# Performance work log

Hardware: AMD Instinct MI355X
Metric: run time of the kernel (lower is better)

Reference implementation:

```python
import jax, jax.numpy as jnp
import numpy as np

N_PTS = 600000; N_VOX = 250000; N_PART = 125000; N_NEXT = 100000; N_DS = 100000
C = 64; K = 27; B = 2; SX, SY, SZ = 240, 180, 16


def leaky(x):
    return jnp.where(x >= 0, x, 0.1 * x)


def bn(x, g, b, eps=1e-5):
    # training-mode BatchNorm1d: batch stats over the row dim
    mu = x.mean(0)
    var = x.var(0)
    return (x - mu) * jax.lax.rsqrt(var + eps) * g + b


def subm_conv(x, nbr, W):
    # submanifold 3x3x3 conv via precomputed neighbor map: [N,K] gather + per-offset GEMM
    return jnp.einsum('nkc,kcd->nd', x[nbr], W)


def basic_block(x, nbr, W1, g1, b1, W2, g2, b2):
    h = leaky(bn(subm_conv(x, nbr, W1), g1, b1))
    h = bn(subm_conv(h, nbr, W2), g2, b2)
    return leaky(h + x)


def scatter_mean(x, idx, n):
    s = jax.ops.segment_sum(x, idx, num_segments=n)
    cnt = jax.ops.segment_sum(jnp.ones((x.shape[0], 1), x.dtype), idx, num_segments=n)
    return s / jnp.maximum(cnt, 1.0)


def forward(feats, feats_part, Wv11, g11, b11, Wv12, g12, b12, Wv21, g21, b21, Wv22, g22, b22, Wlog, blog, Wi, bi, Wp1, bp1, gp1, bp1n, Wp2, bp2, gp2, bp2n, Wp3, bp3, Wo1, bo1, Wo2, bo2, nbr, nbr_part, coors, coors_inv_last, coors_inv_next, ds_inv):
    # v_enc: two SparseBasicBlocks (shared weights for full and partial tensors)
    v = basic_block(basic_block(feats, nbr, Wv11, g11, b11, Wv12, g12, b12), nbr, Wv21, g21, b21, Wv22, g22, b22)
    vp = basic_block(basic_block(feats_part, nbr_part, Wv11, g11, b11, Wv12, g12, b12), nbr_part, Wv21, g21, b21, Wv22, g22, b22)
    # mae logits on partial tensor + dense BCEWithLogits against all-ones occupancy
    logit = subm_conv(vp, nbr_part, Wlog) + blog  # [N_PART, 1]
    ncell = B * SX * SY * SZ
    flat = ((coors[:, 0] * SX + coors[:, 1]) * SY + coors[:, 2]) * SZ + coors[:, 3]
    x_dense = jnp.zeros((ncell,), feats.dtype).at[flat[:N_PART]].set(logit[:, 0])
    t_dense = jnp.zeros((ncell,), feats.dtype).at[flat].set(1.0)
    loss = jnp.mean(jnp.maximum(x_dense, 0.0) - x_dense * t_dense + jnp.log1p(jnp.exp(-jnp.abs(x_dense))))
    # point_encoder on sparse feats + voxel feats
    feat_sum = feats + v
    ds = scatter_mean(feat_sum, ds_inv, N_DS)           # downsample via unique-inverse
    identity = leaky(feat_sum @ Wi + bi)                # layer_in
    h = bn(leaky(ds @ Wp1 + bp1), gp1, bp1n)            # PPmodel
    h = bn(leaky(h @ Wp2 + bp2), gp2, bp2n)
    h = leaky(h @ Wp3 + bp3)
    cat = jnp.concatenate([identity, h[ds_inv]], axis=1)  # [N_VOX, 2C]
    g = cat[coors_inv_last]                             # gather to points [N_PTS, 2C]
    lo = leaky(g @ Wo1 + bo1) @ Wo2 + bo2               # layer_out
    p_fea = scatter_mean(lo, coors_inv_next, N_NEXT)    # [N_NEXT, C]
    return p_fea[coors_inv_next], loss


def setup_inputs():
    key = jax.random.key(0)
    ks = iter(jax.random.split(key, 48))
    f32 = jnp.float32
    def rn(shape, s):
        return jax.random.normal(next(ks), shape, f32) * s
    def ri(shape, hi):
        return jax.random.randint(next(ks), shape, 0, hi, jnp.int32)
    d = {}
    d['feats'] = rn((N_VOX, C), 1.0)
    d['feats_part'] = rn((N_PART, C), 1.0)
    for nm in ('Wv11', 'Wv12', 'Wv21', 'Wv22'):
        d[nm] = rn((K, C, C), 0.02)
    for nm in ('g11', 'g12', 'g21', 'g22'):
        d[nm] = jnp.ones((C,), f32)
    for nm in ('b11', 'b12', 'b21', 'b22'):
        d[nm] = jnp.zeros((C,), f32)
    d['Wlog'] = rn((K, C, 1), 0.02); d['blog'] = jnp.zeros((1,), f32)
    d['Wi'] = rn((C, C), 0.1); d['bi'] = jnp.zeros((C,), f32)
    d['Wp1'] = rn((C, C // 2), 0.1); d['bp1'] = jnp.zeros((C // 2,), f32)
    d['gp1'] = jnp.ones((C // 2,), f32); d['bp1n'] = jnp.zeros((C // 2,), f32)
    d['Wp2'] = rn((C // 2, C // 2), 0.15); d['bp2'] = jnp.zeros((C // 2,), f32)
    d['gp2'] = jnp.ones((C // 2,), f32); d['bp2n'] = jnp.zeros((C // 2,), f32)
    d['Wp3'] = rn((C // 2, C), 0.15); d['bp3'] = jnp.zeros((C,), f32)
    d['Wo1'] = rn((2 * C, C), 0.08); d['bo1'] = jnp.zeros((C,), f32)
    d['Wo2'] = rn((C, C), 0.1); d['bo2'] = jnp.zeros((C,), f32)
    d['nbr'] = ri((N_VOX, K), N_VOX)
    d['nbr_part'] = ri((N_PART, K), N_PART)
    d['coors'] = jnp.stack([ri((N_VOX,), B), ri((N_VOX,), SX), ri((N_VOX,), SY), ri((N_VOX,), SZ)], axis=1)
    d['coors_inv_last'] = ri((N_PTS,), N_VOX)
    d['coors_inv_next'] = ri((N_PTS,), N_NEXT)
    d['ds_inv'] = ri((N_VOX,), N_DS)
    return d


def reference(feats, feats_part, Wv11, g11, b11, Wv12, g12, b12, Wv21, g21, b21, Wv22, g22, b22, Wlog, blog, Wi, bi, Wp1, bp1, gp1, bp1n, Wp2, bp2, gp2, bp2n, Wp3, bp3, Wo1, bo1, Wo2, bo2, nbr, nbr_part, coors, coors_inv_last, coors_inv_next, ds_inv):
    return forward(feats, feats_part, Wv11, g11, b11, Wv12, g12, b12, Wv21, g21, b21, Wv22, g22, b22, Wlog, blog, Wi, bi, Wp1, bp1, gp1, bp1n, Wp2, bp2, gp2, bp2n, Wp3, bp3, Wo1, bo1, Wo2, bo2, nbr, nbr_part, coors, coors_inv_last, coors_inv_next, ds_inv)
```

## Files before the change

### kernel.cpp

```cpp
#include <hip/hip_runtime.h>
#include <math.h>

#define NVOX 250000
#define NPART 125000
#define NPTS 600000
#define NNEXT 100000
#define NDS 100000
#define NCELL 1382400

static __device__ __forceinline__ float lk(float x) { return x >= 0.f ? x : 0.1f * x; }

static __device__ __forceinline__ unsigned short f2bf(float f) {
    unsigned u = __float_as_uint(f);
    unsigned r = (u + 0x7FFFu + ((u >> 16) & 1u)) >> 16;
    return (unsigned short)r;
}
static __device__ __forceinline__ unsigned short f2h(float f) {
    _Float16 h = (_Float16)f;
    return *(unsigned short*)&h;
}
static __device__ __forceinline__ float h2f(unsigned short u) {
    _Float16 h = *(_Float16*)&u;
    return (float)h;
}

typedef short v8s __attribute__((ext_vector_type(8)));
typedef _Float16 v8h __attribute__((ext_vector_type(8)));
typedef float v4f __attribute__((ext_vector_type(4)));
#define MFMAH __builtin_amdgcn_mfma_f32_16x16x32_f16

static __device__ __forceinline__ float* lob_row(float* r0, float* r1, float* r2, int row) {
    if (row < 200000) return r0 + (size_t)row * 64;
    if (row < 500000) return r1 + (size_t)(row - 200000) * 64;
    return r2 + (size_t)(row - 500000) * 64;
}

__global__ void fill_u32_kernel(unsigned* __restrict__ p, unsigned v, long n) {
    long i = (long)blockIdx.x * 256 + threadIdx.x;
    if (i < n) p[i] = v;
}

__global__ void wsplit_kernel(const float* __restrict__ W, unsigned short* __restrict__ hi,
                              unsigned short* __restrict__ lo) {
    int i = blockIdx.x * 256 + threadIdx.x;
    if (i < 27 * 4096) {
        int k = i >> 12, rem = i & 4095, d = rem >> 6, c = rem & 63;
        float w = W[k * 4096 + c * 64 + d];
        unsigned short h = f2h(w);
        hi[i] = h;
        lo[i] = f2h(w - h2f(h));
    }
}

__global__ void xhalf_kernel(const float* __restrict__ X, unsigned short* __restrict__ out, long n) {
    long i = (long)blockIdx.x * 256 + threadIdx.x;
    if (i < n) out[i] = f2h(X[i]);
}

__global__ __launch_bounds__(256) void conv_mfma_kernel(
    const unsigned short* __restrict__ Xh,
    const int* __restrict__ nbr,
    const unsigned short* __restrict__ Wthi, const unsigned short* __restrict__ Wtlo,
    float* __restrict__ Y, float* __restrict__ stats, int N)
{
    __shared__ __align__(16) unsigned short Wlds[2][8192];

    const int t = threadIdx.x;
    const int wave = t >> 6, lane = t & 63;
    const int m = lane & 15, q = lane >> 4;
    const int qo = q * 8;
    const long base = (long)blockIdx.x * 128 + wave * 32;

    long r0 = base + m;
    long r1 = base + 16 + m;
    long r0c = r0 < N ? r0 : (long)(N - 1);
    long r1c = r1 < N ? r1 : (long)(N - 1);
    const long o0g = r0c * 27, o1g = r1c * 27;

    const int zb = wave * 4096 + lane * 16;
    const int z0 = zb, z1 = zb + 1024, z2 = zb + 2048, z3 = zb + 3072;
    const int d0 = z0 ^ (((z0 >> 7) & 7) << 4);
    const int d1 = z1 ^ (((z1 >> 7) & 7) << 4);
    const int d2 = z2 ^ (((z2 >> 7) & 7) << 4);
    const int d3 = z3 ^ (((z3 >> 7) & 7) << 4);

    v4f acc[2][4];
    #pragma unroll
    for (int s = 0; s < 2; ++s)
        #pragma unroll
        for (int c = 0; c < 4; ++c)
            acc[s][c] = (v4f){0.f, 0.f, 0.f, 0.f};

    {
        const char* ghb = (const char*)Wthi;
        const char* glb = (const char*)Wtlo;
        v8s w0 = *(const v8s*)(z0 < 8192 ? ghb + z0 : glb + (z0 - 8192));
        v8s w1 = *(const v8s*)(z1 < 8192 ? ghb + z1 : glb + (z1 - 8192));
        v8s w2 = *(const v8s*)(z2 < 8192 ? ghb + z2 : glb + (z2 - 8192));
        v8s w3 = *(const v8s*)(z3 < 8192 ? ghb + z3 : glb + (z3 - 8192));
        char* lb = (char*)&Wlds[0][0];
        *(v8s*)(lb + d0) = w0; *(v8s*)(lb + d1) = w1;
        *(v8s*)(lb + d2) = w2; *(v8s*)(lb + d3) = w3;
    }
    __syncthreads();

    #pragma unroll 1
    for (int k = 0; k < 27; ++k) {
        const int cb = k & 1;
        const bool st = (k + 1 < 27);
        v8s w0, w1, w2, w3;
        if (st) {
            const char* ghb = (const char*)(Wthi + (size_t)(k + 1) * 4096);
            const char* glb = (const char*)(Wtlo + (size_t)(k + 1) * 4096);
            w0 = *(const v8s*)(z0 < 8192 ? ghb + z0 : glb + (z0 - 8192));
            w1 = *(const v8s*)(z1 < 8192 ? ghb + z1 : glb + (z1 - 8192));
            w2 = *(const v8s*)(z2 < 8192 ? ghb + z2 : glb + (z2 - 8192));
            w3 = *(const v8s*)(z3 < 8192 ? ghb + z3 : glb + (z3 - 8192));
        }
        int j0 = nbr[o0g + k];
        int j1 = nbr[o1g + k];
        const unsigned short* x0 = Xh + (size_t)j0 * 64;
        const unsigned short* x1 = Xh + (size_t)j1 * 64;
        v8h a00 = *(const v8h*)(x0 + qo);
        v8h a01 = *(const v8h*)(x0 + 32 + qo);
        v8h a10 = *(const v8h*)(x1 + qo);
        v8h a11 = *(const v8h*)(x1 + 32 + qo);
        const char* wb = (const char*)&Wlds[cb][0];
        const int sw = (m & 7) << 4;
        #pragma unroll
        for (int ct = 0; ct < 4; ++ct) {
            const int rowoff = (ct * 16 + m) * 128;
            v8h bh0 = *(const v8h*)(wb + rowoff + ((q * 16) ^ sw));
            v8h bh1 = *(const v8h*)(wb + rowoff + ((q * 16 + 64) ^ sw));
            v8h bl0 = *(const v8h*)(wb + 8192 + rowoff + ((q * 16) ^ sw));
            v8h bl1 = *(const v8h*)(wb + 8192 + rowoff + ((q * 16 + 64) ^ sw));
            acc[0][ct] = MFMAH(a00, bh0, acc[0][ct], 0, 0, 0);
            acc[0][ct] = MFMAH(a01, bh1, acc[0][ct], 0, 0, 0);
            acc[0][ct] = MFMAH(a00, bl0, acc[0][ct], 0, 0, 0);
            acc[0][ct] = MFMAH(a01, bl1, acc[0][ct], 0, 0, 0);
            acc[1][ct] = MFMAH(a10, bh0, acc[1][ct], 0, 0, 0);
            acc[1][ct] = MFMAH(a11, bh1, acc[1][ct], 0, 0, 0);
            acc[1][ct] = MFMAH(a10, bl0, acc[1][ct], 0, 0, 0);
            acc[1][ct] = MFMAH(a11, bl1, acc[1][ct], 0, 0, 0);
        }
        if (st) {
            char* lb = (char*)&Wlds[1 - cb][0];
            *(v8s*)(lb + d0) = w0; *(v8s*)(lb + d1) = w1;
            *(v8s*)(lb + d2) = w2; *(v8s*)(lb + d3) = w3;
        }
        __syncthreads();
    }

    #pragma unroll
    for (int s = 0; s < 2; ++s)
        #pragma unroll
        for (int ct = 0; ct < 4; ++ct)
            #pragma unroll
            for (int rg = 0; rg < 4; ++rg) {
                long r = base + s * 16 + q * 4 + rg;
                if (r < N) Y[r * 64 + ct * 16 + m] = acc[s][ct][rg];
            }

    float* shred = (float*)&Wlds[0][0];
    if (t < 128) shred[t] = 0.f;
    __syncthreads();
    #pragma unroll
    for (int ct = 0; ct < 4; ++ct) {
        float s = 0.f, s2 = 0.f;
        #pragma unroll
        for (int ss = 0; ss < 2; ++ss)
            #pragma unroll
            for (int rg = 0; rg < 4; ++rg) {
                long r = base + ss * 16 + q * 4 + rg;
                if (r < N) { float v = acc[ss][ct][rg]; s += v; s2 += v * v; }
            }
        atomicAdd(&shred[ct * 16 + m], s);
        atomicAdd(&shred[64 + ct * 16 + m], s2);
    }
    __syncthreads();
    if (t < 64) {
        atomicAdd(&stats[t], shred[t]);
        atomicAdd(&stats[64 + t], shred[64 + t]);
    }
}

template<int CC>
__global__ __launch_bounds__(256) void colstats_kernel(const float* __restrict__ Y, int N, float* __restrict__ stats) {
    constexpr int RG = 256 / CC;
    const int t = threadIdx.x;
    const int c = t % CC, rg = t / CC;
    float s = 0.f, s2 = 0.f;
    for (long r = (long)blockIdx.x * RG + rg; r < N; r += (long)gridDim.x * RG) {
        float v = Y[r * CC + c];
        s += v; s2 += v * v;
    }
    __shared__ float sh[256], sh2[256];
    sh[t] = s; sh2[t] = s2;
    __syncthreads();
    if (t < CC) {
        #pragma unroll
        for (int g = 1; g < RG; ++g) { s += sh[g * CC + t]; s2 += sh2[g * CC + t]; }
        atomicAdd(&stats[t], s);
        atomicAdd(&stats[CC + t], s2);
    }
}

__global__ void mkscale_kernel(float* __restrict__ stats, const float* __restrict__ g,
                               const float* __restrict__ b, float invN, int CC) {
    int c = threadIdx.x;
    if (c < CC) {
        float mu = stats[c] * invN;
        float var = stats[CC + c] * invN - mu * mu;
        float sc = g[c] * rsqrtf(var + 1e-5f);
        stats[2 * CC + c] = sc;
        stats[3 * CC + c] = b[c] - mu * sc;
    }
}

template<int CC, int MODE, int PAIR, int WOUT>
__global__ __launch_bounds__(256) void apply_bn_kernel(
    const float* __restrict__ Yin, const float* __restrict__ stats,
    const float* __restrict__ res, const float* __restrict__ res2,
    float* __restrict__ out, unsigned short* __restrict__ ohalf, long n4)
{
    long i = (long)blockIdx.x * 256 + threadIdx.x;
    if (i >= n4) return;
    int c4 = (int)(i % (CC / 4)) * 4;
    float4 y = ((const float4*)Yin)[i];
    float4 sc = *(const float4*)(stats + 2 * CC + c4);
    float4 sf = *(const float4*)(stats + 3 * CC + c4);
    float x0 = y.x * sc.x + sf.x;
    float x1 = y.y * sc.y + sf.y;
    float x2 = y.z * sc.z + sf.z;
    float x3 = y.w * sc.w + sf.w;
    if (MODE >= 2) {
        float4 rr = ((const float4*)res)[i];
        x0 += rr.x; x1 += rr.y; x2 += rr.z; x3 += rr.w;
    }
    if (MODE >= 1) { x0 = lk(x0); x1 = lk(x1); x2 = lk(x2); x3 = lk(x3); }
    if (MODE == 3) {
        float4 rr2 = ((const float4*)res2)[i];
        x0 += rr2.x; x1 += rr2.y; x2 += rr2.z; x3 += rr2.w;
    }
    if (WOUT) ((float4*)out)[i] = make_float4(x0, x1, x2, x3);
    if (PAIR) {
        ushort4 h;
        h.x = f2h(x0); h.y = f2h(x1); h.z = f2h(x2); h.w = f2h(x3);
        *(ushort4*)(ohalf + i * 4) = h;
    }
}

template<int CIN, int COUT, int ACT>
__global__ __launch_bounds__(256) void gemm_kernel(
    const float* __restrict__ X, const float* __restrict__ W,
    const float* __restrict__ bias, float* __restrict__ Y, int N)
{
    constexpr int TX = COUT / 4;
    constexpr int TY = 256 / TX;
    constexpr int ROWS = TY * 4;
    constexpr int CHUNK = (CIN < 64) ? CIN : 64;
    constexpr int NCH = CIN / CHUNK;
    __shared__ float XsT[CHUNK][ROWS + 4];
    __shared__ float Ws[CHUNK][COUT + 4];
    const int t = threadIdx.x;
    const int row0 = blockIdx.x * ROWS;
    const int ty = t / TX, tx = t % TX;
    float acc[4][4] = {{0.f}};
    for (int cc = 0; cc < NCH; ++cc) {
        __syncthreads();
        for (int i = t * 4; i < CHUNK * COUT; i += 1024) {
            int c = i / COUT, d = i % COUT;
            *(float4*)&Ws[c][d] = *(const float4*)(W + (size_t)(cc * CHUNK + c) * COUT + d);
        }
        for (int i = t * 4; i < ROWS * CHUNK; i += 1024) {
            int r = i / CHUNK, c0 = i % CHUNK;
            int gr = row0 + r;
            float4 v = make_float4(0.f, 0.f, 0.f, 0.f);
            if (gr < N) v = *(const float4*)(X + (size_t)gr * CIN + cc * CHUNK + c0);
            XsT[c0 + 0][r] = v.x; XsT[c0 + 1][r] = v.y; XsT[c0 + 2][r] = v.z; XsT[c0 + 3][r] = v.w;
        }
        __syncthreads();
        #pragma unroll 8
        for (int c = 0; c < CHUNK; ++c) {
            float4 xv = *(const float4*)&XsT[c][ty * 4];
            float4 wv = *(const float4*)&Ws[c][tx * 4];
            acc[0][0] += xv.x * wv.x; acc[0][1] += xv.x * wv.y; acc[0][2] += xv.x * wv.z; acc[0][3] += xv.x * wv.w;
            acc[1][0] += xv.y * wv.x; acc[1][1] += xv.y * wv.y; acc[1][2] += xv.y * wv.z; acc[1][3] += xv.y * wv.w;
            acc[2][0] += xv.z * wv.x; acc[2][1] += xv.z * wv.y; acc[2][2] += xv.z * wv.z; acc[2][3] += xv.z * wv.w;
            acc[3][0] += xv.w * wv.x; acc[3][1] += xv.w * wv.y; acc[3][2] += xv.w * wv.z; acc[3][3] += xv.w * wv.w;
        }
    }
    float4 bv = *(const float4*)(bias + tx * 4);
    #pragma unroll
    for (int i2 = 0; i2 < 4; ++i2) {
        int gr = row0 + ty * 4 + i2;
        if (gr < N) {
            float o0 = acc[i2][0] + bv.x, o1 = acc[i2][1] + bv.y;
            float o2 = acc[i2][2] + bv.z, o3 = acc[i2][3] + bv.w;
            if (ACT) { o0 = lk(o0); o1 = lk(o1); o2 = lk(o2); o3 = lk(o3); }
            *(float4*)(Y + (size_t)gr * COUT + tx * 4) = make_float4(o0, o1, o2, o3);
        }
    }
}

__global__ void hist_kernel(const int* __restrict__ idx, int* __restrict__ cnt, int n) {
    int i = blockIdx.x * 256 + threadIdx.x;
    if (i < n) atomicAdd(&cnt[idx[i]], 1);
}

__global__ void scan_reduce_kernel(const int* __restrict__ cnt, int* __restrict__ bsum, int T) {
    __shared__ int sh[256];
    const int b = blockIdx.x, t = threadIdx.x;
    int s = 0;
    #pragma unroll
    for (int u = 0; u < 4; ++u) {
        int i = b * 1024 + u * 256 + t;
        if (i < T) s += cnt[i];
    }
    sh[t] = s; __syncthreads();
    for (int st = 128; st > 0; st >>= 1) { if (t < st) sh[t] += sh[t + st]; __syncthreads(); }
    if (t == 0) bsum[b] = sh[0];
}

__global__ void scan_top_kernel(int* __restrict__ bsum, int nb) {
    __shared__ int sh[256];
    const int t = threadIdx.x;
    sh[t] = (t < nb) ? bsum[t] : 0;
    __syncthreads();
    if (t == 0) {
        int run = 0;
        for (int i = 0; i < nb; ++i) { int v = sh[i]; sh[i] = run; run += v; }
    }
    __syncthreads();
    if (t < nb) bsum[t] = sh[t];
}

__global__ void scan_final_kernel(const int* __restrict__ cnt, const int* __restrict__ bsum,
                                  int* __restrict__ offs, int* __restrict__ cursor, int T) {
    __shared__ int sh[256];
    const int b = blockIdx.x, t = threadIdx.x;
    const int i0 = b * 1024 + t * 4;
    int v0 = 0, v1 = 0, v2 = 0, v3 = 0;
    if (i0 + 0 < T) v0 = cnt[i0 + 0];
    if (i0 + 1 < T) v1 = cnt[i0 + 1];
    if (i0 + 2 < T) v2 = cnt[i0 + 2];
    if (i0 + 3 < T) v3 = cnt[i0 + 3];
    const int tot = v0 + v1 + v2 + v3;
    sh[t] = tot; __syncthreads();
    for (int st = 1; st < 256; st <<= 1) {
        int x = (t >= st) ? sh[t - st] : 0;
        __syncthreads();
        sh[t] += x;
        __syncthreads();
    }
    int ex = sh[t] - tot + bsum[b];
    if (i0 + 0 < T) { offs[i0 + 0] = ex; cursor[i0 + 0] = ex; } ex += v0;
    if (i0 + 1 < T) { offs[i0 + 1] = ex; cursor[i0 + 1] = ex; } ex += v1;
    if (i0 + 2 < T) { offs[i0 + 2] = ex; cursor[i0 + 2] = ex; } ex += v2;
    if (i0 + 3 < T) { offs[i0 + 3] = ex; cursor[i0 + 3] = ex; }
}

__global__ void place_kernel(const int* __restrict__ idx, int* __restrict__ cursor,
                             int* __restrict__ perm, int n) {
    int i = blockIdx.x * 256 + threadIdx.x;
    if (i < n) { int p = atomicAdd(&cursor[idx[i]], 1); perm[p] = i; }
}

__global__ __launch_bounds__(256) void segmean_kernel(
    const float* __restrict__ src, const int* __restrict__ perm,
    const int* __restrict__ offs, const int* __restrict__ cnt,
    float* __restrict__ dst, int T)
{
    const int wave = threadIdx.x >> 6, lane = threadIdx.x & 63;
    const int tg = blockIdx.x * 4 + wave;
    if (tg >= T) return;
    const int o = offs[tg], c = cnt[tg];
    float acc = 0.f;
    for (int j = 0; j < c; ++j) {
        int r = perm[o + j];
        acc += src[(size_t)r * 64 + lane];
    }
    dst[(size_t)tg * 64 + lane] = acc / fmaxf((float)c, 1.0f);
}

__global__ __launch_bounds__(256) void segmean_lob_kernel(
    float* __restrict__ l0, float* __restrict__ l1, float* __restrict__ l2,
    const int* __restrict__ perm, const int* __restrict__ offs, const int* __restrict__ cnt,
    float* __restrict__ dst, int T)
{
    const int wave = threadIdx.x >> 6, lane = threadIdx.x & 63;
    const int tg = blockIdx.x * 4 + wave;
    if (tg >= T) return;
    const int o = offs[tg], c = cnt[tg];
    float acc = 0.f;
    for (int j = 0; j < c; ++j) {
        int r = perm[o + j];
        acc += lob_row(l0, l1, l2, r)[lane];
    }
    dst[(size_t)tg * 64 + lane] = acc / fmaxf((float)c, 1.0f);
}

__global__ __launch_bounds__(256) void layer_out_fused_kernel(
    const float* __restrict__ iden, const float* __restrict__ h3,
    const int* __restrict__ cil, const int* __restrict__ dsinv,
    const float* __restrict__ Wo1, const float* __restrict__ bo1,
    const float* __restrict__ Wo2, const float* __restrict__ bo2,
    float* __restrict__ lob0, float* __restrict__ lob1, float* __restrict__ lob2, int N)
{
    __shared__ float XsT[64][68];
    __shared__ float Ws[64][68];
    const int t = threadIdx.x;
    const int row0 = blockIdx.x * 64;
    const int ty = t >> 4, tx = t & 15;
    const int lr = t >> 2, ls = t & 3;
    const int gr = row0 + lr;
    int v = (gr < N) ? cil[gr] : 0;
    int vds = dsinv[v];
    float acc[4][4] = {{0.f}};
    for (int cc = 0; cc < 2; ++cc) {
        const float* src = (cc == 0) ? (iden + (size_t)v * 64) : (h3 + (size_t)vds * 64);
        const float* xr = src + ls * 16;
        float4 v0 = *(const float4*)(xr);
        float4 v1 = *(const float4*)(xr + 4);
        float4 v2f = *(const float4*)(xr + 8);
        float4 v3 = *(const float4*)(xr + 12);
        const float* Wk = Wo1 + (size_t)cc * 4096;
        float4 w0 = *(const float4*)(Wk + t * 4);
        float4 w1 = *(const float4*)(Wk + t * 4 + 1024);
        float4 w2 = *(const float4*)(Wk + t * 4 + 2048);
        float4 w3 = *(const float4*)(Wk + t * 4 + 3072);
        __syncthreads();
        {
            int i0 = t * 4;
            *(float4*)&Ws[i0 >> 6][i0 & 63] = w0; i0 += 1024;
            *(float4*)&Ws[i0 >> 6][i0 & 63] = w1; i0 += 1024;
            *(float4*)&Ws[i0 >> 6][i0 & 63] = w2; i0 += 1024;
            *(float4*)&Ws[i0 >> 6][i0 & 63] = w3;
        }
        const int cb = ls * 16;
        XsT[cb + 0][lr] = v0.x; XsT[cb + 1][lr] = v0.y; XsT[cb + 2][lr] = v0.z; XsT[cb + 3][lr] = v0.w;
        XsT[cb + 4][lr] = v1.x; XsT[cb + 5][lr] = v1.y; XsT[cb + 6][lr] = v1.z; XsT[cb + 7][lr] = v1.w;
        XsT[cb + 8][lr] = v2f.x; XsT[cb + 9][lr] = v2f.y; XsT[cb + 10][lr] = v2f.z; XsT[cb + 11][lr] = v2f.w;
        XsT[cb + 12][lr] = v3.x; XsT[cb + 13][lr] = v3.y; XsT[cb + 14][lr] = v3.z; XsT[cb + 15][lr] = v3.w;
        __syncthreads();
        #pragma unroll 16
        for (int c = 0; c < 64; ++c) {
            float4 xv = *(const float4*)&XsT[c][ty * 4];
            float4 wv = *(const float4*)&Ws[c][tx * 4];
            acc[0][0] += xv.x * wv.x; acc[0][1] += xv.x * wv.y; acc[0][2] += xv.x * wv.z; acc[0][3] += xv.x * wv.w;
            acc[1][0] += xv.y * wv.x; acc[1][1] += xv.y * wv.y; acc[1][2] += xv.y * wv.z; acc[1][3] += xv.y * wv.w;
            acc[2][0] += xv.z * wv.x; acc[2][1] += xv.z * wv.y; acc[2][2] += xv.z * wv.z; acc[2][3] += xv.z * wv.w;
            acc[3][0] += xv.w * wv.x; acc[3][1] += xv.w * wv.y; acc[3][2] += xv.w * wv.z; acc[3][3] += xv.w * wv.w;
        }
    }
    float4 u0 = *(const float4*)(Wo2 + t * 4);
    float4 u1 = *(const float4*)(Wo2 + t * 4 + 1024);
    float4 u2 = *(const float4*)(Wo2 + t * 4 + 2048);
    float4 u3 = *(const float4*)(Wo2 + t * 4 + 3072);
    float4 b1v = *(const float4*)(bo1 + tx * 4);
    __syncthreads();
    {
        int i0 = t * 4;
        *(float4*)&Ws[i0 >> 6][i0 & 63] = u0; i0 += 1024;
        *(float4*)&Ws[i0 >> 6][i0 & 63] = u1; i0 += 1024;
        *(float4*)&Ws[i0 >> 6][i0 & 63] = u2; i0 += 1024;
        *(float4*)&Ws[i0 >> 6][i0 & 63] = u3;
    }
    #pragma unroll
    for (int i = 0; i < 4; ++i) {
        XsT[tx * 4 + 0][ty * 4 + i] = lk(acc[i][0] + b1v.x);
        XsT[tx * 4 + 1][ty * 4 + i] = lk(acc[i][1] + b1v.y);
        XsT[tx * 4 + 2][ty * 4 + i] = lk(acc[i][2] + b1v.z);
        XsT[tx * 4 + 3][ty * 4 + i] = lk(acc[i][3] + b1v.w);
    }
    __syncthreads();
    float acc2[4][4] = {{0.f}};
    #pragma unroll 16
    for (int c = 0; c < 64; ++c) {
        float4 xv = *(const float4*)&XsT[c][ty * 4];
        float4 wv = *(const float4*)&Ws[c][tx * 4];
        acc2[0][0] += xv.x * wv.x; acc2[0][1] += xv.x * wv.y; acc2[0][2] += xv.x * wv.z; acc2[0][3] += xv.x * wv.w;
        acc2[1][0] += xv.y * wv.x; acc2[1][1] += xv.y * wv.y; acc2[1][2] += xv.y * wv.z; acc2[1][3] += xv.y * wv.w;
        acc2[2][0] += xv.z * wv.x; acc2[2][1] += xv.z * wv.y; acc2[2][2] += xv.z * wv.z; acc2[2][3] += xv.z * wv.w;
        acc2[3][0] += xv.w * wv.x; acc2[3][1] += xv.w * wv.y; acc2[3][2] += xv.w * wv.z; acc2[3][3] += xv.w * wv.w;
    }
    float4 b2v = *(const float4*)(bo2 + tx * 4);
    #pragma unroll
    for (int i2 = 0; i2 < 4; ++i2) {
        int gr2 = row0 + ty * 4 + i2;
        if (gr2 < N) {
            float* dst = lob_row(lob0, lob1, lob2, gr2) + tx * 4;
            *(float4*)dst = make_float4(acc2[i2][0] + b2v.x, acc2[i2][1] + b2v.y,
                                        acc2[i2][2] + b2v.z, acc2[i2][3] + b2v.w);
        }
    }
}

__global__ void gather_out_kernel(const float* __restrict__ pf, const int* __restrict__ cin,
                                  float* __restrict__ out, int N) {
    long i = (long)blockIdx.x * 256 + threadIdx.x;
    if (i < (long)N * 16) {
        int p = (int)(i >> 4), q = (int)(i & 15);
        ((float4*)out)[i] = *(const float4*)(pf + (size_t)cin[p] * 64 + q * 4);
    }
}

__global__ __launch_bounds__(256) void slog_kernel(
    const float* __restrict__ Cp, const float* __restrict__ Wlog,
    float* __restrict__ s, int N)
{
    __shared__ float CpS[64][65];
    __shared__ float WlS[27][65];
    const int t = threadIdx.x;
    const int j0 = blockIdx.x * 64;
    for (int i = t; i < 1728; i += 256) WlS[i / 64][i % 64] = Wlog[i];
    for (int i = t; i < 1024; i += 256) {
        int r = i >> 4, c4 = (i & 15) * 4;
        int gj = j0 + r;
        float4 v = make_float4(0.f, 0.f, 0.f, 0.f);
        if (gj < N) v = *(const float4*)(Cp + (size_t)gj * 64 + c4);
        CpS[r][c4 + 0] = v.x; CpS[r][c4 + 1] = v.y; CpS[r][c4 + 2] = v.z; CpS[r][c4 + 3] = v.w;
    }
    __syncthreads();
    for (int i = t; i < 64 * 27; i += 256) {
        int r = i / 27, k = i % 27;
        int gj = j0 + r;
        if (gj < N) {
            float acc = 0.f;
            #pragma unroll 16
            for (int c = 0; c < 64; ++c) acc += CpS[r][c] * WlS[k][c];
            s[(size_t)gj * 27 + k] = acc;
        }
    }
}

__global__ void logit_gather_kernel(const float* __restrict__ s, const int* __restrict__ nbrp,
                                    const float* __restrict__ blog, float* __restrict__ out, int N) {
    int n = blockIdx.x * 256 + threadIdx.x;
    if (n < N) {
        float acc = blog[0];
        #pragma unroll
        for (int k = 0; k < 27; ++k) {
            int j = nbrp[(size_t)n * 27 + k];
            acc += s[(size_t)j * 27 + k];
        }
        out[n] = acc;
    }
}

__global__ void loss_scatter1_kernel(const int* __restrict__ coors, int* __restrict__ tflag,
                                     int* __restrict__ winner, int N, int NP) {
    int n = blockIdx.x * 256 + threadIdx.x;
    if (n < N) {
        int b = coors[n * 4], x = coors[n * 4 + 1], y = coors[n * 4 + 2], z = coors[n * 4 + 3];
        int flat = ((b * 240 + x) * 180 + y) * 16 + z;
        tflag[flat] = 1;
        if (n < NP) atomicMax(&winner[flat], n);
    }
}

__global__ void loss_scatter2_kernel(const int* __restrict__ coors, const int* __restrict__ winner,
                                     const float* __restrict__ logit, float* __restrict__ xdense, int NP) {
    int n = blockIdx.x * 256 + threadIdx.x;
    if (n < NP) {
        int b = coors[n * 4], x = coors[n * 4 + 1], y = coors[n * 4 + 2], z = coors[n * 4 + 3];
        int flat = ((b * 240 + x) * 180 + y) * 16 + z;
        if (winner[flat] == n) xdense[flat] = logit[n];
    }
}

__global__ void loss_reduce_kernel(const float* __restrict__ xdense, const int* __restrict__ tflag,
                                   float* __restrict__ accum) {
    int i = blockIdx.x * 256 + threadIdx.x;
    float x = xdense[i];
    float tt = (float)tflag[i];
    float term = fmaxf(x, 0.f) - x * tt + log1pf(expf(-fabsf(x)));
    __shared__ float sh[256];
    sh[threadIdx.x] = term;
    __syncthreads();
    for (int s = 128; s > 0; s >>= 1) {
        if (threadIdx.x < s) sh[threadIdx.x] += sh[threadIdx.x + s];
        __syncthreads();
    }
    if (threadIdx.x == 0) atomicAdd(accum, sh[0]);
}

__global__ void loss_final_kernel(const float* __restrict__ accum, float* __restrict__ out) {
    out[0] = accum[0] / (float)NCELL;
}

extern "C" void kernel_launch(void* const* d_in, const int* in_sizes, int n_in,
                              void* d_out, int out_size, void* d_ws, size_t ws_size,
                              hipStream_t stream)
{
    const float* feats  = (const float*)d_in[0];
    const float* featsp = (const float*)d_in[1];
    const float* Wv11 = (const float*)d_in[2];
    const float* Wv12 = (const float*)d_in[3];
    const float* Wv21 = (const float*)d_in[4];
    const float* Wv22 = (const float*)d_in[5];
    const float* g11 = (const float*)d_in[6];
    const float* g12 = (const float*)d_in[7];
    const float* g21 = (const float*)d_in[8];
    const float* g22 = (const float*)d_in[9];
    const float* b11 = (const float*)d_in[10];
    const float* b12 = (const float*)d_in[11];
    const float* b21 = (const float*)d_in[12];
    const float* b22 = (const float*)d_in[13];
    const float* Wlog = (const float*)d_in[14];
    const float* blog = (const float*)d_in[15];
    const float* Wi  = (const float*)d_in[16];
    const float* bi  = (const float*)d_in[17];
    const float* Wp1 = (const float*)d_in[18];
    const float* bp1 = (const float*)d_in[19];
    const float* gp1 = (const float*)d_in[20];
    const float* bp1n = (const float*)d_in[21];
    const float* Wp2 = (const float*)d_in[22];
    const float* bp2 = (const float*)d_in[23];
    const float* gp2 = (const float*)d_in[24];
    const float* bp2n = (const float*)d_in[25];
    const float* Wp3 = (const float*)d_in[26];
    const float* bp3 = (const float*)d_in[27];
    const float* Wo1 = (const float*)d_in[28];
    const float* bo1 = (const float*)d_in[29];
    const float* Wo2 = (const float*)d_in[30];
    const float* bo2 = (const float*)d_in[31];
    const int* nbr   = (const int*)d_in[32];
    const int* nbrp  = (const int*)d_in[33];
    const int* coors = (const int*)d_in[34];
    const int* cil   = (const int*)d_in[35];
    const int* cin   = (const int*)d_in[36];
    const int* dsinv = (const int*)d_in[37];
    (void)in_sizes; (void)n_in; (void)out_size; (void)ws_size;

    float* ws = (float*)d_ws;
    float* A     = ws;
    float* H     = ws + 16000000L;
    float* Hpf32 = ws + 32000000L;
    float* lob2  = ws + 32000000L;
    int* perm_cin   = (int*)(ws + 38400000L);
    int* offs_cin   = (int*)(ws + 39000000L);
    int* cursor_cin = (int*)(ws + 39100000L);
    int* cnt_cin    = (int*)(ws + 39200000L);
    int* perm_ds    = (int*)(ws + 39300000L);
    int* offs_ds    = (int*)(ws + 39550000L);
    int* cursor_ds  = (int*)(ws + 39650000L);
    int* cnt_ds     = (int*)(ws + 39750000L);
    int* bsum       = (int*)(ws + 39850000L);
    float* psum  = ws + 40000000L;
    float* slog  = psum;
    unsigned short* wt = (unsigned short*)(ws + 46500000L);
    float* stats = ws + 46950000L;
    float* lacc  = ws + 46952560L;
    unsigned short* wh11 = wt + 0L * 110592;
    unsigned short* wl11 = wt + 1L * 110592;
    unsigned short* wh12 = wt + 2L * 110592;
    unsigned short* wl12 = wt + 3L * 110592;
    unsigned short* wh21 = wt + 4L * 110592;
    unsigned short* wl21 = wt + 5L * 110592;
    unsigned short* wh22 = wt + 6L * 110592;
    unsigned short* wl22 = wt + 7L * 110592;

    float* o = (float*)d_out;
    unsigned short* F0 = (unsigned short*)(o);
    unsigned short* F1 = (unsigned short*)(o + 8000000L);
    unsigned short* P0 = (unsigned short*)(o);
    unsigned short* P1 = (unsigned short*)(o + 4000000L);
    float* Cp = o + 16000000L;
    float* xdense = o + 32000000L;
    int*   tflag  = (int*)(o + 33382400L);
    int*   winner = (int*)(o + 34764800L);
    float* logitb = o + 36147200L;
    float* dssum = o;
    float* t1b   = o + 6400000L;
    float* t2b   = o + 9600000L;
    float* h3b   = o + 12800000L;
    float* lob0 = o;
    float* lob1 = o + 19200000L;
    float* out = (float*)d_out;

    auto cdiv = [](long a, long b) { return (unsigned)((a + b - 1) / b); };
    dim3 B256(256);

    fill_u32_kernel<<<cdiv(2561, 256), B256, 0, stream>>>((unsigned*)stats, 0u, 2561);
    fill_u32_kernel<<<cdiv(2764800, 256), B256, 0, stream>>>((unsigned*)xdense, 0u, 2764800);
    fill_u32_kernel<<<cdiv(1382400, 256), B256, 0, stream>>>((unsigned*)winner, 0xFFFFFFFFu, 1382400);

    wsplit_kernel<<<432, B256, 0, stream>>>(Wv11, wh11, wl11);
    wsplit_kernel<<<432, B256, 0, stream>>>(Wv12, wh12, wl12);
    wsplit_kernel<<<432, B256, 0, stream>>>(Wv21, wh21, wl21);
    wsplit_kernel<<<432, B256, 0, stream>>>(Wv22, wh22, wl22);

    xhalf_kernel<<<cdiv(16000000, 256), B256, 0, stream>>>(feats, F0, 16000000L);
    conv_mfma_kernel<<<cdiv(NVOX, 128), B256, 0, stream>>>(F0, nbr, wh11, wl11, A, stats + 0 * 256, NVOX);
    mkscale_kernel<<<1, 64, 0, stream>>>(stats + 0 * 256, g11, b11, 1.0f / NVOX, 64);
    apply_bn_kernel<64, 1, 1, 0><<<cdiv(NVOX * 16L, 256), B256, 0, stream>>>(A, stats + 0 * 256, nullptr, nullptr, nullptr, F1, NVOX * 16L);
    conv_mfma_kernel<<<cdiv(NVOX, 128), B256, 0, stream>>>(F1, nbr, wh12, wl12, A, stats + 1 * 256, NVOX);
    mkscale_kernel<<<1, 64, 0, stream>>>(stats + 1 * 256, g12, b12, 1.0f / NVOX, 64);
    apply_bn_kernel<64, 2, 1, 1><<<cdiv(NVOX * 16L, 256), B256, 0, stream>>>(A, stats + 1 * 256, feats, nullptr, H, F0, NVOX * 16L);
    conv_mfma_kernel<<<cdiv(NVOX, 128), B256, 0, stream>>>(F0, nbr, wh21, wl21, A, stats + 2 * 256, NVOX);
    mkscale_kernel<<<1, 64, 0, stream>>>(stats + 2 * 256, g21, b21, 1.0f / NVOX, 64);
    apply_bn_kernel<64, 1, 1, 0><<<cdiv(NVOX * 16L, 256), B256, 0, stream>>>(A, stats + 2 * 256, nullptr, nullptr, nullptr, F1, NVOX * 16L);
    conv_mfma_kernel<<<cdiv(NVOX, 128), B256, 0, stream>>>(F1, nbr, wh22, wl22, A, stats + 3 * 256, NVOX);
    mkscale_kernel<<<1, 64, 0, stream>>>(stats + 3 * 256, g22, b22, 1.0f / NVOX, 64);
    apply_bn_kernel<64, 3, 0, 1><<<cdiv(NVOX * 16L, 256), B256, 0, stream>>>(A, stats + 3 * 256, H, feats, H, nullptr, NVOX * 16L);

    xhalf_kernel<<<cdiv(8000000, 256), B256, 0, stream>>>(featsp, P0, 8000000L);
    conv_mfma_kernel<<<cdiv(NPART, 128), B256, 0, stream>>>(P0, nbrp, wh11, wl11, A, stats + 4 * 256, NPART);
    mkscale_kernel<<<1, 64, 0, stream>>>(stats + 4 * 256, g11, b11, 1.0f / NPART, 64);
    apply_bn_kernel<64, 1, 1, 0><<<cdiv(NPART * 16L, 256), B256, 0, stream>>>(A, stats + 4 * 256, nullptr, nullptr, nullptr, P1, NPART * 16L);
    conv_mfma_kernel<<<cdiv(NPART, 128), B256, 0, stream>>>(P1, nbrp, wh12, wl12, A, stats + 5 * 256, NPART);
    mkscale_kernel<<<1, 64, 0, stream>>>(stats + 5 * 256, g12, b12, 1.0f / NPART, 64);
    apply_bn_kernel<64, 2, 1, 1><<<cdiv(NPART * 16L, 256), B256, 0, stream>>>(A, stats + 5 * 256, featsp, nullptr, Hpf32, P0, NPART * 16L);
    conv_mfma_kernel<<<cdiv(NPART, 128), B256, 0, stream>>>(P0, nbrp, wh21, wl21, A, stats + 6 * 256, NPART);
    mkscale_kernel<<<1, 64, 0, stream>>>(stats + 6 * 256, g21, b21, 1.0f / NPART, 64);
    apply_bn_kernel<64, 1, 1, 0><<<cdiv(NPART * 16L, 256), B256, 0, stream>>>(A, stats + 6 * 256, nullptr, nullptr, nullptr, P1, NPART * 16L);
    conv_mfma_kernel<<<cdiv(NPART, 128), B256, 0, stream>>>(P1, nbrp, wh22, wl22, A, stats + 7 * 256, NPART);
    mkscale_kernel<<<1, 64, 0, stream>>>(stats + 7 * 256, g22, b22, 1.0f / NPART, 64);
    apply_bn_kernel<64, 2, 0, 1><<<cdiv(NPART * 16L, 256), B256, 0, stream>>>(A, stats + 7 * 256, Hpf32, nullptr, Cp, nullptr, NPART * 16L);

    slog_kernel<<<cdiv(NPART, 64), B256, 0, stream>>>(Cp, Wlog, slog, NPART);
    logit_gather_kernel<<<cdiv(NPART, 256), B256, 0, stream>>>(slog, nbrp, blog, logitb, NPART);
    loss_scatter1_kernel<<<cdiv(NVOX, 256), B256, 0, stream>>>(coors, tflag, winner, NVOX, NPART);
    loss_scatter2_kernel<<<cdiv(NPART, 256), B256, 0, stream>>>(coors, winner, logitb, xdense, NPART);
    loss_reduce_kernel<<<NCELL / 256, B256, 0, stream>>>(xdense, tflag, lacc);

    fill_u32_kernel<<<cdiv(100000, 256), B256, 0, stream>>>((unsigned*)cnt_cin, 0u, 100000);
    fill_u32_kernel<<<cdiv(100000, 256), B256, 0, stream>>>((unsigned*)cnt_ds, 0u, 100000);
    hist_kernel<<<cdiv(NPTS, 256), B256, 0, stream>>>(cin, cnt_cin, NPTS);
    hist_kernel<<<cdiv(NVOX, 256), B256, 0, stream>>>(dsinv, cnt_ds, NVOX);
    scan_reduce_kernel<<<98, B256, 0, stream>>>(cnt_cin, bsum, 100000);
    scan_top_kernel<<<1, B256, 0, stream>>>(bsum, 98);
    scan_final_kernel<<<98, B256, 0, stream>>>(cnt_cin, bsum, offs_cin, cursor_cin, 100000);
    scan_reduce_kernel<<<98, B256, 0, stream>>>(cnt_ds, bsum, 100000);
    scan_top_kernel<<<1, B256, 0, stream>>>(bsum, 98);
    scan_final_kernel<<<98, B256, 0, stream>>>(cnt_ds, bsum, offs_ds, cursor_ds, 100000);
    place_kernel<<<cdiv(NPTS, 256), B256, 0, stream>>>(cin, cursor_cin, perm_cin, NPTS);
    place_kernel<<<cdiv(NVOX, 256), B256, 0, stream>>>(dsinv, cursor_ds, perm_ds, NVOX);

    segmean_kernel<<<cdiv(NDS, 4), B256, 0, stream>>>(H, perm_ds, offs_ds, cnt_ds, dssum, NDS);
    gemm_kernel<64, 64, 1><<<cdiv(NVOX, 64), B256, 0, stream>>>(H, Wi, bi, A, NVOX);

    gemm_kernel<64, 32, 1><<<cdiv(NDS, 128), B256, 0, stream>>>(dssum, Wp1, bp1, t1b, NDS);
    colstats_kernel<32><<<256, B256, 0, stream>>>(t1b, NDS, stats + 8 * 256);
    mkscale_kernel<<<1, 64, 0, stream>>>(stats + 8 * 256, gp1, bp1n, 1.0f / NDS, 32);
    apply_bn_kernel<32, 0, 0, 1><<<cdiv((long)NDS * 8, 256), B256, 0, stream>>>(t1b, stats + 8 * 256, nullptr, nullptr, t1b, nullptr, (long)NDS * 8);

    gemm_kernel<32, 32, 1><<<cdiv(NDS, 128), B256, 0, stream>>>(t1b, Wp2, bp2, t2b, NDS);
    colstats_kernel<32><<<256, B256, 0, stream>>>(t2b, NDS, stats + 9 * 256);
    mkscale_kernel<<<1, 64, 0, stream>>>(stats + 9 * 256, gp2, bp2n, 1.0f / NDS, 32);
    apply_bn_kernel<32, 0, 0, 1><<<cdiv((long)NDS * 8, 256), B256, 0, stream>>>(t2b, stats + 9 * 256, nullptr, nullptr, t2b, nullptr, (long)NDS * 8);

    gemm_kernel<32, 64, 1><<<cdiv(NDS, 64), B256, 0, stream>>>(t2b, Wp3, bp3, h3b, NDS);

    layer_out_fused_kernel<<<cdiv(NPTS, 64), B256, 0, stream>>>(A, h3b, cil, dsinv, Wo1, bo1, Wo2, bo2, lob0, lob1, lob2, NPTS);
    segmean_lob_kernel<<<cdiv(NNEXT, 4), B256, 0, stream>>>(lob0, lob1, lob2, perm_cin, offs_cin, cnt_cin, psum, NNEXT);

    gather_out_kernel<<<cdiv((long)NPTS * 16, 256), B256, 0, stream>>>(psum, cin, out, NPTS);
    loss_final_kernel<<<1, 1, 0, stream>>>(lacc, out + 38400000L);
}
```

Baseline: 2.508 ms.

## Run layer_out MLP on fp16 MFMA with split weights and half-precision inputs

Replaces the scalar FP32 layer_out kernel with an MFMA version that uses 16x16x32 f16 instructions. Weights are split into hi/lo fp16 parts to keep accuracy. The identity and h3 producers now write fp16 rows, which halves the gather traffic for the 600k-point layer. The cost is precision loss on the activations, which are rounded to fp16, plus a per-wave LDS stage for the hidden activations.

After: 2.426 ms. 1.03x faster.

```diff
diff --git a/kernel.cpp b/kernel.cpp
--- a/kernel.cpp
+++ b/kernel.cpp
@@ -10,11 +10,6 @@
 
 static __device__ __forceinline__ float lk(float x) { return x >= 0.f ? x : 0.1f * x; }
 
-static __device__ __forceinline__ unsigned short f2bf(float f) {
-    unsigned u = __float_as_uint(f);
-    unsigned r = (u + 0x7FFFu + ((u >> 16) & 1u)) >> 16;
-    return (unsigned short)r;
-}
 static __device__ __forceinline__ unsigned short f2h(float f) {
     _Float16 h = (_Float16)f;
     return *(unsigned short*)&h;
@@ -46,6 +41,30 @@
     if (i < 27 * 4096) {
         int k = i >> 12, rem = i & 4095, d = rem >> 6, c = rem & 63;
         float w = W[k * 4096 + c * 64 + d];
+        unsigned short h = f2h(w);
+        hi[i] = h;
+        lo[i] = f2h(w - h2f(h));
+    }
+}
+
+__global__ void wsplit_o1_kernel(const float* __restrict__ W, unsigned short* __restrict__ hi,
+                                 unsigned short* __restrict__ lo) {
+    int i = blockIdx.x * 256 + threadIdx.x;
+    if (i < 8192) {
+        int d = i >> 7, kk = i & 127;
+        float w = W[kk * 64 + d];
+        unsigned short h = f2h(w);
+        hi[i] = h;
+        lo[i] = f2h(w - h2f(h));
+    }
+}
+
+__global__ void wsplit_o2_kernel(const float* __restrict__ W, unsigned short* __restrict__ hi,
+                                 unsigned short* __restrict__ lo) {
+    int i = blockIdx.x * 256 + threadIdx.x;
+    if (i < 4096) {
+        int d = i >> 6, kk = i & 63;
+        float w = W[kk * 64 + d];
         unsigned short h = f2h(w);
         hi[i] = h;
         lo[i] = f2h(w - h2f(h));
@@ -250,10 +269,10 @@
     }
 }
 
-template<int CIN, int COUT, int ACT>
+template<int CIN, int COUT, int ACT, int H16>
 __global__ __launch_bounds__(256) void gemm_kernel(
     const float* __restrict__ X, const float* __restrict__ W,
-    const float* __restrict__ bias, float* __restrict__ Y, int N)
+    const float* __restrict__ bias, void* __restrict__ Yv, int N)
 {
     constexpr int TX = COUT / 4;
     constexpr int TY = 256 / TX;
@@ -298,7 +317,13 @@
             float o0 = acc[i2][0] + bv.x, o1 = acc[i2][1] + bv.y;
             float o2 = acc[i2][2] + bv.z, o3 = acc[i2][3] + bv.w;
             if (ACT) { o0 = lk(o0); o1 = lk(o1); o2 = lk(o2); o3 = lk(o3); }
-            *(float4*)(Y + (size_t)gr * COUT + tx * 4) = make_float4(o0, o1, o2, o3);
+            if (H16) {
+                ushort4 h;
+                h.x = f2h(o0); h.y = f2h(o1); h.z = f2h(o2); h.w = f2h(o3);
+                *(ushort4*)((unsigned short*)Yv + (size_t)gr * COUT + tx * 4) = h;
+            } else {
+                *(float4*)((float*)Yv + (size_t)gr * COUT + tx * 4) = make_float4(o0, o1, o2, o3);
+            }
         }
     }
 }
@@ -400,98 +425,105 @@
     dst[(size_t)tg * 64 + lane] = acc / fmaxf((float)c, 1.0f);
 }
 
-__global__ __launch_bounds__(256) void layer_out_fused_kernel(
-    const float* __restrict__ iden, const float* __restrict__ h3,
+__global__ __launch_bounds__(256) void layer_out_mfma_kernel(
+    const unsigned short* __restrict__ Ah,
+    const unsigned short* __restrict__ h3h,
     const int* __restrict__ cil, const int* __restrict__ dsinv,
-    const float* __restrict__ Wo1, const float* __restrict__ bo1,
-    const float* __restrict__ Wo2, const float* __restrict__ bo2,
+    const unsigned short* __restrict__ W1hi, const unsigned short* __restrict__ W1lo,
+    const unsigned short* __restrict__ W2hi, const unsigned short* __restrict__ W2lo,
+    const float* __restrict__ bo1, const float* __restrict__ bo2,
     float* __restrict__ lob0, float* __restrict__ lob1, float* __restrict__ lob2, int N)
 {
-    __shared__ float XsT[64][68];
-    __shared__ float Ws[64][68];
+    __shared__ __align__(16) _Float16 W1s[2][64][136];
+    __shared__ __align__(16) _Float16 W2s[2][64][72];
+    __shared__ __align__(16) _Float16 hs[4][16][72];
+
     const int t = threadIdx.x;
-    const int row0 = blockIdx.x * 64;
-    const int ty = t >> 4, tx = t & 15;
-    const int lr = t >> 2, ls = t & 3;
-    const int gr = row0 + lr;
-    int v = (gr < N) ? cil[gr] : 0;
+    for (int i = t; i < 1024; i += 256) {
+        int r = i >> 4, c8 = (i & 15) * 8;
+        *(v8h*)&W1s[0][r][c8] = *(const v8h*)(W1hi + r * 128 + c8);
+        *(v8h*)&W1s[1][r][c8] = *(const v8h*)(W1lo + r * 128 + c8);
+    }
+    for (int i = t; i < 512; i += 256) {
+        int r = i >> 3, c8 = (i & 7) * 8;
+        *(v8h*)&W2s[0][r][c8] = *(const v8h*)(W2hi + r * 64 + c8);
+        *(v8h*)&W2s[1][r][c8] = *(const v8h*)(W2lo + r * 64 + c8);
+    }
+    __syncthreads();
+
+    const int wave = t >> 6, lane = t & 63;
+    const int m = lane & 15, q = lane >> 4;
+    const int row0 = blockIdx.x * 64 + wave * 16;
+
+    int gr = row0 + m;
+    int grc = gr < N ? gr : N - 1;
+    int v = cil[grc];
     int vds = dsinv[v];
-    float acc[4][4] = {{0.f}};
-    for (int cc = 0; cc < 2; ++cc) {
-        const float* src = (cc == 0) ? (iden + (size_t)v * 64) : (h3 + (size_t)vds * 64);
-        const float* xr = src + ls * 16;
-        float4 v0 = *(const float4*)(xr);
-        float4 v1 = *(const float4*)(xr + 4);
-        float4 v2f = *(const float4*)(xr + 8);
-        float4 v3 = *(const float4*)(xr + 12);
-        const float* Wk = Wo1 + (size_t)cc * 4096;
-        float4 w0 = *(const float4*)(Wk + t * 4);
-        float4 w1 = *(const float4*)(Wk + t * 4 + 1024);
-        float4 w2 = *(const float4*)(Wk + t * 4 + 2048);
-        float4 w3 = *(const float4*)(Wk + t * 4 + 3072);
-        __syncthreads();
-        {
-            int i0 = t * 4;
-            *(float4*)&Ws[i0 >> 6][i0 & 63] = w0; i0 += 1024;
-            *(float4*)&Ws[i0 >> 6][i0 & 63] = w1; i0 += 1024;
-            *(float4*)&Ws[i0 >> 6][i0 & 63] = w2; i0 += 1024;
-            *(float4*)&Ws[i0 >> 6][i0 & 63] = w3;
-        }
-        const int cb = ls * 16;
-        XsT[cb + 0][lr] = v0.x; XsT[cb + 1][lr] = v0.y; XsT[cb + 2][lr] = v0.z; XsT[cb + 3][lr] = v0.w;
-        XsT[cb + 4][lr] = v1.x; XsT[cb + 5][lr] = v1.y; XsT[cb + 6][lr] = v1.z; XsT[cb + 7][lr] = v1.w;
-        XsT[cb + 8][lr] = v2f.x; XsT[cb + 9][lr] = v2f.y; XsT[cb + 10][lr] = v2f.z; XsT[cb + 11][lr] = v2f.w;
-        XsT[cb + 12][lr] = v3.x; XsT[cb + 13][lr] = v3.y; XsT[cb + 14][lr] = v3.z; XsT[cb + 15][lr] = v3.w;
-        __syncthreads();
-        #pragma unroll 16
-        for (int c = 0; c < 64; ++c) {
-            float4 xv = *(const float4*)&XsT[c][ty * 4];
-            float4 wv = *(const float4*)&Ws[c][tx * 4];
-            acc[0][0] += xv.x * wv.x; acc[0][1] += xv.x * wv.y; acc[0][2] += xv.x * wv.z; acc[0][3] += xv.x * wv.w;
-            acc[1][0] += xv.y * wv.x; acc[1][1] += xv.y * wv.y; acc[1][2] += xv.y * wv.z; acc[1][3] += xv.y * wv.w;
-            acc[2][0] += xv.z * wv.x; acc[2][1] += xv.z * wv.y; acc[2][2] += xv.z * wv.z; acc[2][3] += xv.z * wv.w;
-            acc[3][0] += xv.w * wv.x; acc[3][1] += xv.w * wv.y; acc[3][2] += xv.w * wv.z; acc[3][3] += xv.w * wv.w;
-        }
-    }
-    float4 u0 = *(const float4*)(Wo2 + t * 4);
-    float4 u1 = *(const float4*)(Wo2 + t * 4 + 1024);
-    float4 u2 = *(const float4*)(Wo2 + t * 4 + 2048);
-    float4 u3 = *(const float4*)(Wo2 + t * 4 + 3072);
-    float4 b1v = *(const float4*)(bo1 + tx * 4);
-    __syncthreads();
-    {
-        int i0 = t * 4;
-        *(float4*)&Ws[i0 >> 6][i0 & 63] = u0; i0 += 1024;
-        *(float4*)&Ws[i0 >> 6][i0 & 63] = u1; i0 += 1024;
-        *(float4*)&Ws[i0 >> 6][i0 & 63] = u2; i0 += 1024;
-        *(float4*)&Ws[i0 >> 6][i0 & 63] = u3;
-    }
-    #pragma unroll
-    for (int i = 0; i < 4; ++i) {
-        XsT[tx * 4 + 0][ty * 4 + i] = lk(acc[i][0] + b1v.x);
-        XsT[tx * 4 + 1][ty * 4 + i] = lk(acc[i][1] + b1v.y);
-        XsT[tx * 4 + 2][ty * 4 + i] = lk(acc[i][2] + b1v.z);
-        XsT[tx * 4 + 3][ty * 4 + i] = lk(acc[i][3] + b1v.w);
-    }
-    __syncthreads();
-    float acc2[4][4] = {{0.f}};
-    #pragma unroll 16
-    for (int c = 0; c < 64; ++c) {
-        float4 xv = *(const float4*)&XsT[c][ty * 4];
-        float4 wv = *(const float4*)&Ws[c][tx * 4];
-        acc2[0][0] += xv.x * wv.x; acc2[0][1] += xv.x * wv.y; acc2[0][2] += xv.x * wv.z; acc2[0][3] += xv.x * wv.w;
-        acc2[1][0] += xv.y * wv.x; acc2[1][1] += xv.y * wv.y; acc2[1][2] += xv.y * wv.z; acc2[1][3] += xv.y * wv.w;
-        acc2[2][0] += xv.z * wv.x; acc2[2][1] += xv.z * wv.y; acc2[2][2] += xv.z * wv.z; acc2[2][3] += xv.z * wv.w;
-        acc2[3][0] += xv.w * wv.x; acc2[3][1] += xv.w * wv.y; acc2[3][2] += xv.w * wv.z; acc2[3][3] += xv.w * wv.w;
-    }
-    float4 b2v = *(const float4*)(bo2 + tx * 4);
-    #pragma unroll
-    for (int i2 = 0; i2 < 4; ++i2) {
-        int gr2 = row0 + ty * 4 + i2;
-        if (gr2 < N) {
-            float* dst = lob_row(lob0, lob1, lob2, gr2) + tx * 4;
-            *(float4*)dst = make_float4(acc2[i2][0] + b2v.x, acc2[i2][1] + b2v.y,
-                                        acc2[i2][2] + b2v.z, acc2[i2][3] + b2v.w);
+    const unsigned short* arow = Ah + (size_t)v * 64;
+    const unsigned short* hrow = h3h + (size_t)vds * 64;
+    v8h a0 = *(const v8h*)(arow + q * 8);
+    v8h a1 = *(const v8h*)(arow + 32 + q * 8);
+    v8h a2 = *(const v8h*)(hrow + q * 8);
+    v8h a3 = *(const v8h*)(hrow + 32 + q * 8);
+
+    v4f acc1[4];
+    #pragma unroll
+    for (int ct = 0; ct < 4; ++ct) acc1[ct] = (v4f){0.f, 0.f, 0.f, 0.f};
+    #pragma unroll
+    for (int ct = 0; ct < 4; ++ct) {
+        const int d = ct * 16 + m;
+        v8h b0h = *(const v8h*)&W1s[0][d][q * 8];
+        v8h b1h = *(const v8h*)&W1s[0][d][32 + q * 8];
+        v8h b2h = *(const v8h*)&W1s[0][d][64 + q * 8];
+        v8h b3h = *(const v8h*)&W1s[0][d][96 + q * 8];
+        v8h b0l = *(const v8h*)&W1s[1][d][q * 8];
+        v8h b1l = *(const v8h*)&W1s[1][d][32 + q * 8];
+        v8h b2l = *(const v8h*)&W1s[1][d][64 + q * 8];
+        v8h b3l = *(const v8h*)&W1s[1][d][96 + q * 8];
+        acc1[ct] = MFMAH(a0, b0h, acc1[ct], 0, 0, 0);
+        acc1[ct] = MFMAH(a1, b1h, acc1[ct], 0, 0, 0);
+        acc1[ct] = MFMAH(a2, b2h, acc1[ct], 0, 0, 0);
+        acc1[ct] = MFMAH(a3, b3h, acc1[ct], 0, 0, 0);
+        acc1[ct] = MFMAH(a0, b0l, acc1[ct], 0, 0, 0);
+        acc1[ct] = MFMAH(a1, b1l, acc1[ct], 0, 0, 0);
+        acc1[ct] = MFMAH(a2, b2l, acc1[ct], 0, 0, 0);
+        acc1[ct] = MFMAH(a3, b3l, acc1[ct], 0, 0, 0);
+    }
+    #pragma unroll
+    for (int ct = 0; ct < 4; ++ct) {
+        const int col = ct * 16 + m;
+        const float b1 = bo1[col];
+        #pragma unroll
+        for (int rg = 0; rg < 4; ++rg)
+            hs[wave][q * 4 + rg][col] = (_Float16)lk(acc1[ct][rg] + b1);
+    }
+    __syncthreads();
+
+    v8h c0 = *(const v8h*)&hs[wave][m][q * 8];
+    v8h c1 = *(const v8h*)&hs[wave][m][32 + q * 8];
+    v4f acc2[4];
+    #pragma unroll
+    for (int ct = 0; ct < 4; ++ct) acc2[ct] = (v4f){0.f, 0.f, 0.f, 0.f};
+    #pragma unroll
+    for (int ct = 0; ct < 4; ++ct) {
+        const int d = ct * 16 + m;
+        v8h d0h = *(const v8h*)&W2s[0][d][q * 8];
+        v8h d1h = *(const v8h*)&W2s[0][d][32 + q * 8];
+        v8h d0l = *(const v8h*)&W2s[1][d][q * 8];
+        v8h d1l = *(const v8h*)&W2s[1][d][32 + q * 8];
+        acc2[ct] = MFMAH(c0, d0h, acc2[ct], 0, 0, 0);
+        acc2[ct] = MFMAH(c1, d1h, acc2[ct], 0, 0, 0);
+        acc2[ct] = MFMAH(c0, d0l, acc2[ct], 0, 0, 0);
+        acc2[ct] = MFMAH(c1, d1l, acc2[ct], 0, 0, 0);
+    }
+    #pragma unroll
+    for (int ct = 0; ct < 4; ++ct) {
+        const int col = ct * 16 + m;
+        const float b2 = bo2[col];
+        #pragma unroll
+        for (int rg = 0; rg < 4; ++rg) {
+            int r = row0 + q * 4 + rg;
+            if (r < N) lob_row(lob0, lob1, lob2, r)[col] = acc2[ct][rg] + b2;
         }
     }
 }
@@ -635,6 +667,7 @@
 
     float* ws = (float*)d_ws;
     float* A     = ws;
+    unsigned short* Ah = (unsigned short*)ws;
     float* H     = ws + 16000000L;
     float* Hpf32 = ws + 32000000L;
     float* lob2  = ws + 32000000L;
@@ -649,6 +682,11 @@
     int* bsum       = (int*)(ws + 39850000L);
     float* psum  = ws + 40000000L;
     float* slog  = psum;
+    unsigned short* wo = (unsigned short*)(ws + 46400000L);
+    unsigned short* wo1hi = wo;
+    unsigned short* wo1lo = wo + 8192;
+    unsigned short* wo2hi = wo + 16384;
+    unsigned short* wo2lo = wo + 20480;
     unsigned short* wt = (unsigned short*)(ws + 46500000L);
     float* stats = ws + 46950000L;
     float* lacc  = ws + 46952560L;
@@ -674,7 +712,7 @@
     float* dssum = o;
     float* t1b   = o + 6400000L;
     float* t2b   = o + 9600000L;
-    float* h3b   = o + 12800000L;
+    unsigned short* h3h = (unsigned short*)(o + 12800000L);
     float* lob0 = o;
     float* lob1 = o + 19200000L;
     float* out = (float*)d_out;
@@ -690,6 +728,8 @@
     wsplit_kernel<<<432, B256, 0, stream>>>(Wv12, wh12, wl12);
     wsplit_kernel<<<432, B256, 0, stream>>>(Wv21, wh21, wl21);
     wsplit_kernel<<<432, B256, 0, stream>>>(Wv22, wh22, wl22);
+    wsplit_o1_kernel<<<32, B256, 0, stream>>>(Wo1, wo1hi, wo1lo);
+    wsplit_o2_kernel<<<16, B256, 0, stream>>>(Wo2, wo2hi, wo2lo);
 
     xhalf_kernel<<<cdiv(16000000, 256), B256, 0, stream>>>(feats, F0, 16000000L);
     conv_mfma_kernel<<<cdiv(NVOX, 128), B256, 0, stream>>>(F0, nbr, wh11, wl11, A, stats + 0 * 256, NVOX);
@@ -739,21 +779,22 @@
     place_kernel<<<cdiv(NVOX, 256), B256, 0, stream>>>(dsinv, cursor_ds, perm_ds, NVOX);
 
     segmean_kernel<<<cdiv(NDS, 4), B256, 0, stream>>>(H, perm_ds, offs_ds, cnt_ds, dssum, NDS);
-    gemm_kernel<64, 64, 1><<<cdiv(NVOX, 64), B256, 0, stream>>>(H, Wi, bi, A, NVOX);
-
-    gemm_kernel<64, 32, 1><<<cdiv(NDS, 128), B256, 0, stream>>>(dssum, Wp1, bp1, t1b, NDS);
+    gemm_kernel<64, 64, 1, 1><<<cdiv(NVOX, 64), B256, 0, stream>>>(H, Wi, bi, Ah, NVOX);
+
+    gemm_kernel<64, 32, 1, 0><<<cdiv(NDS, 128), B256, 0, stream>>>(dssum, Wp1, bp1, t1b, NDS);
     colstats_kernel<32><<<256, B256, 0, stream>>>(t1b, NDS, stats + 8 * 256);
     mkscale_kernel<<<1, 64, 0, stream>>>(stats + 8 * 256, gp1, bp1n, 1.0f / NDS, 32);
     apply_bn_kernel<32, 0, 0, 1><<<cdiv((long)NDS * 8, 256), B256, 0, stream>>>(t1b, stats + 8 * 256, nullptr, nullptr, t1b, nullptr, (long)NDS * 8);
 
-    gemm_kernel<32, 32, 1><<<cdiv(NDS, 128), B256, 0, stream>>>(t1b, Wp2, bp2, t2b, NDS);
+    gemm_kernel<32, 32, 1, 0><<<cdiv(NDS, 128), B256, 0, stream>>>(t1b, Wp2, bp2, t2b, NDS);
     colstats_kernel<32><<<256, B256, 0, stream>>>(t2b, NDS, stats + 9 * 256);
     mkscale_kernel<<<1, 64, 0, stream>>>(stats + 9 * 256, gp2, bp2n, 1.0f / NDS, 32);
     apply_bn_kernel<32, 0, 0, 1><<<cdiv((long)NDS * 8, 256), B256, 0, stream>>>(t2b, stats + 9 * 256, nullptr, nullptr, t2b, nullptr, (long)NDS * 8);
 
-    gemm_kernel<32, 64, 1><<<cdiv(NDS, 64), B256, 0, stream>>>(t2b, Wp3, bp3, h3b, NDS);
-
-    layer_out_fused_kernel<<<cdiv(NPTS, 64), B256, 0, stream>>>(A, h3b, cil, dsinv, Wo1, bo1, Wo2, bo2, lob0, lob1, lob2, NPTS);
+    gemm_kernel<32, 64, 1, 1><<<cdiv(NDS, 64), B256, 0, stream>>>(t2b, Wp3, bp3, h3h, NDS);
+
+    layer_out_mfma_kernel<<<cdiv(NPTS, 64), B256, 0, stream>>>(Ah, h3h, cil, dsinv,
+        wo1hi, wo1lo, wo2hi, wo2lo, bo1, bo2, lob0, lob1, lob2, NPTS);
     segmean_lob_kernel<<<cdiv(NNEXT, 4), B256, 0, stream>>>(lob0, lob1, lob2, perm_cin, offs_cin, cnt_cin, psum, NNEXT);
 
     gather_out_kernel<<<cdiv((long)NPTS * 16, 256), B256, 0, stream>>>(psum, cin, out, NPTS);
```
